# Kernel tuning notes

Hardware: AMD Instinct MI355X
Metric: run time of the kernel (lower is better)

## Reference

```python
import jax, jax.numpy as jnp
import numpy as np
import math

IMG = 256      # image H = W (img_shape)
N_ANG = 360    # projection views over [0, pi)
N_DET = 256    # radial detector bins
N_SAMP = 256   # samples along each ray
VOX = 2.0      # voxel size / detector bin width in mm (isotropic)
FWHM = 4.0     # gaussian_PSF FWHM in mm


def _gauss_kernel(sigma):
    radius = max(1, int(math.ceil(3.0 * sigma)))
    t = np.arange(-radius, radius + 1, dtype=np.float64)
    k = np.exp(-0.5 * (t / sigma) ** 2)
    return (k / k.sum()).astype(np.float32), radius


def _blur_axis(x, sigma, axis):
    """1-D Gaussian blur with reflect padding along `axis` (static small kernel)."""
    k, r = _gauss_kernel(sigma)
    x = jnp.moveaxis(x, axis, -1)
    L = x.shape[-1]
    pad = [(0, 0)] * (x.ndim - 1) + [(r, r)]
    xp = jnp.pad(x, pad, mode='reflect')
    out = sum(float(k[i]) * xp[..., i:i + L] for i in range(2 * r + 1))
    return jnp.moveaxis(out, -1, axis)


def _blur2d(x, sigma):
    return _blur_axis(_blur_axis(x, sigma, -1), sigma, -2)


def _geometry():
    """Static parallel-beam ray-sampling geometry (bilinear taps, in pixel units)."""
    theta = np.pi * np.arange(N_ANG) / N_ANG
    r = (np.arange(N_DET) - (N_DET - 1) / 2.0) * VOX   # detector offsets [mm]
    s = (np.arange(N_SAMP) - (N_SAMP - 1) / 2.0) * VOX  # depth along ray [mm]
    cos = np.cos(theta)[:, None, None]
    sin = np.sin(theta)[:, None, None]
    x = r[None, :, None] * cos - s[None, None, :] * sin  # (A, D, S) mm
    y = r[None, :, None] * sin + s[None, None, :] * cos
    ix = x / VOX + (IMG - 1) / 2.0
    iy = y / VOX + (IMG - 1) / 2.0
    valid = ((ix >= 0) & (ix <= IMG - 1) & (iy >= 0) & (iy <= IMG - 1)).astype(np.float32)
    j0 = np.clip(np.floor(ix).astype(np.int32), 0, IMG - 2)
    i0 = np.clip(np.floor(iy).astype(np.int32), 0, IMG - 2)
    fx = (ix - j0).astype(np.float32)
    fy = (iy - i0).astype(np.float32)
    return i0, j0, fy, fx, valid

_GEO = tuple(jnp.asarray(a) for a in _geometry())


def _project(img):
    """Parallel-view 2D ray projection: img (B,H,W) -> sinogram (B, N_DET, N_ANG)."""
    i0, j0, fy, fx, valid = _GEO
    v00 = img[:, i0, j0]
    v01 = img[:, i0, j0 + 1]
    v10 = img[:, i0 + 1, j0]
    v11 = img[:, i0 + 1, j0 + 1]
    vals = ((1 - fy) * (1 - fx) * v00 + (1 - fy) * fx * v01
            + fy * (1 - fx) * v10 + fy * fx * v11) * valid
    sino = vals.sum(-1) * VOX          # (B, N_ANG, N_DET), line integral in mm
    return jnp.transpose(sino, (0, 2, 1))  # (B, N_DET, N_ANG)


def setup_inputs() -> dict:
    key = jax.random.key(0)
    k1, k2 = jax.random.split(key)
    image = jax.random.uniform(k1, (2, 1, IMG, IMG), dtype=jnp.float32)
    attenuation_map = jax.random.uniform(k2, (2, 1, IMG, IMG), dtype=jnp.float32)
    return {"image": image, "attenuation_map": attenuation_map}


def reference(image, attenuation_map):
    sqrt_log2 = math.sqrt(math.log(2.0))
    sigma_img = (FWHM / (4.0 * sqrt_log2)) / VOX
    # emission PSF blur (reflect) then project
    img_b = _blur2d(image, sigma_img)
    sino = _project(img_b[:, 0])[:, None]          # (B,1,N_DET,N_ANG)
    # attenuation: wider PSF blur, 0.01 scale, project, exponential scaling
    sigma_att = (FWHM / (2.0 * sqrt_log2)) / VOX
    att_b = _blur2d(attenuation_map, sigma_att) * 0.01
    att_sino = _project(att_b[:, 0])[:, None]
    sino = sino * jnp.exp(-att_sino * VOX)
    # column-wise (detector axis) sinogram PSF
    sino = _blur_axis(sino, sigma_img, -2)
    return sino
```

## Files before the change

kernel.cpp:

```cpp
#include <hip/hip_runtime.h>
#include <math.h>

#define IMG 256
#define N_ANG 360
#define N_DET 256

#define NH_BLOCKS 181
#define NV_BLOCKS (179 * 32)
#define EPS 1e-3f

struct W9 { float w[9]; };
struct AngTab { double c, sn; float cf, snf; float pad0, pad1; };

typedef _Float16 h2 __attribute__((ext_vector_type(2)));

#if __has_builtin(__builtin_amdgcn_fdot2)
__device__ __forceinline__ float fdot2(h2 a, h2 b, float c) {
    return __builtin_amdgcn_fdot2(a, b, c, false);
}
#else
__device__ __forceinline__ float fdot2(h2 a, h2 b, float c) {
    return c + (float)a[0] * (float)b[0] + (float)a[1] * (float)b[1];
}
#endif

__device__ __forceinline__ h2 as_h2(unsigned u) { return __builtin_bit_cast(h2, u); }
__device__ __forceinline__ unsigned pack2(float a, float b) {
    h2 v = { (_Float16)a, (_Float16)b };
    return __builtin_bit_cast(unsigned, v);
}
__device__ __forceinline__ unsigned prm(unsigned hi, unsigned lo, unsigned sel) {
#if __has_builtin(__builtin_amdgcn_perm)
    return __builtin_amdgcn_perm(hi, lo, sel);
#else
    unsigned long long cat = ((unsigned long long)hi << 32) | lo;
    unsigned r = 0;
    for (int i = 0; i < 4; ++i) r |= ((unsigned)(cat >> (8 * ((sel >> (8 * i)) & 7))) & 0xff) << (8 * i);
    return r;
#endif
}

__device__ __forceinline__ int refl(int i, int L) {
    if (i < 0) i = -i;
    if (i >= L) i = 2 * (L - 1) - i;
    return i;
}

__global__ void blurpix_k(const float* __restrict__ img, const float* __restrict__ att,
                          uint2* __restrict__ pix, AngTab* __restrict__ tab,
                          W9 wi, W9 wa) {
    int x = threadIdx.x, y = blockIdx.x;
    int gid = y * IMG + x;
    if (gid < N_ANG) {
        double th = M_PI * (double)gid / 360.0;
        double c = cos(th), sn = sin(th);
        AngTab tb;
        tb.c = c; tb.sn = sn; tb.cf = (float)c; tb.snf = (float)sn;
        tb.pad0 = 0.f; tb.pad1 = 0.f;
        tab[gid] = tb;
    }
    float v[4];
    #pragma unroll
    for (int m = 0; m < 4; ++m) {
        const float* src = ((m & 1) ? att : img) + (m >> 1) * IMG * IMG;
        const float* w = (m & 1) ? wa.w : wi.w;
        float acc = 0.f;
        for (int dy = -4; dy <= 4; ++dy) {
            float wy = w[dy + 4];
            if (wy == 0.f) continue;
            const float* rowp = src + refl(y + dy, IMG) * IMG;
            float ra = 0.f;
            for (int dx = -4; dx <= 4; ++dx) ra += w[dx + 4] * rowp[refl(x + dx, IMG)];
            acc += wy * ra;
        }
        v[m] = acc * ((m & 1) ? 0.01f : 1.0f);
    }
    uint2 o;
    o.x = pack2(v[0], v[1]);
    o.y = pack2(v[2], v[3]);
    pix[gid] = o;
}

template <typename P>
__device__ __forceinline__ int lastTrue(P p) {
    if (!p(0)) return -1;
    if (p(255)) return 255;
    int lo = 0, hi = 255;
    while (lo < hi) { int m = (lo + hi + 1) >> 1; if (p(m)) lo = m; else hi = m - 1; }
    return lo;
}
template <typename P>
__device__ __forceinline__ int firstTrue(P p) {
    if (!p(255)) return 256;
    if (p(0)) return 0;
    int lo = 0, hi = 255;
    while (lo < hi) { int m = (lo + hi) >> 1; if (p(m)) hi = m; else lo = m + 1; }
    return lo;
}

__device__ __forceinline__ void tap_acc(const uint2* __restrict__ pix,
                                        int i0, int j0,
                                        float w00, float w01, float w10, float w11,
                                        float4& acc) {
    h2 wt = { (_Float16)w00, (_Float16)w01 };
    h2 wb = { (_Float16)w10, (_Float16)w11 };
    const uint2* p0 = pix + (i0 << 8) + j0;
    uint4 T = *(const uint4*)p0;
    uint4 B = *(const uint4*)(p0 + IMG);
    unsigned ti0 = prm(T.z, T.x, 0x05040100);
    unsigned ta0 = prm(T.z, T.x, 0x07060302);
    unsigned ti1 = prm(T.w, T.y, 0x05040100);
    unsigned ta1 = prm(T.w, T.y, 0x07060302);
    unsigned bi0 = prm(B.z, B.x, 0x05040100);
    unsigned ba0 = prm(B.z, B.x, 0x07060302);
    unsigned bi1 = prm(B.w, B.y, 0x05040100);
    unsigned ba1 = prm(B.w, B.y, 0x07060302);
    acc.x = fdot2(as_h2(ti0), wt, acc.x);
    acc.x = fdot2(as_h2(bi0), wb, acc.x);
    acc.y = fdot2(as_h2(ta0), wt, acc.y);
    acc.y = fdot2(as_h2(ba0), wb, acc.y);
    acc.z = fdot2(as_h2(ti1), wt, acc.z);
    acc.z = fdot2(as_h2(bi1), wb, acc.z);
    acc.w = fdot2(as_h2(ta1), wt, acc.w);
    acc.w = fdot2(as_h2(ba1), wb, acc.w);
}

__global__ __launch_bounds__(512) void proj_k(const uint2* __restrict__ pix,
                                              const AngTab* __restrict__ tab,
                                              float4* __restrict__ part4,
                                              float* __restrict__ out, W9 wblur) {
    int t = threadIdx.x;
    int bx = blockIdx.x;

    if (bx < NH_BLOCKS) {
        int d = t & 255, kc = t >> 8;
        int a = (bx <= 90) ? bx : bx + 179;
        AngTab tb = tab[a];
        double rr = (double)(2 * d - 255);
        double rc = __dmul_rn(rr, tb.c), rs = __dmul_rn(rr, tb.sn);

        auto evIx = [&](int k) -> double {
            double ss = (double)(2 * k - 255);
            return __dadd_rn(__dmul_rn(__dsub_rn(rc, __dmul_rn(ss, tb.sn)), 0.5), 127.5);
        };
        auto evIy = [&](int k) -> double {
            double ss = (double)(2 * k - 255);
            return __dadd_rn(__dmul_rn(__dadd_rn(rs, __dmul_rn(ss, tb.c)), 0.5), 127.5);
        };
        int khiA = lastTrue([&](int k) { return evIx(k) >= 0.0; });
        int kloA = firstTrue([&](int k) { return evIx(k) <= 255.0; });
        int kloB, khiB;
        if (tb.c > 0.0) {
            kloB = firstTrue([&](int k) { return evIy(k) >= 0.0; });
            khiB = lastTrue([&](int k) { return evIy(k) <= 255.0; });
        } else {
            khiB = lastTrue([&](int k) { return evIy(k) >= 0.0; });
            kloB = firstTrue([&](int k) { return evIy(k) <= 255.0; });
        }
        int lo = max(kloA, kloB), hi = min(khiA, khiB);
        lo = max(lo, kc * 128); hi = min(hi, kc * 128 + 127);
        if (lo > hi) { lo = 0; hi = -1; }

        int jl = (hi >= lo) ? lo : 0x7fffffff;
        int jh = (hi >= lo) ? hi : (-0x7fffffff - 1);
        #pragma unroll
        for (int off = 32; off; off >>= 1) {
            jl = min(jl, __shfl_xor(jl, off));
            jh = max(jh, __shfl_xor(jh, off));
        }

        float x0f = (float)evIx(128);
        float y0f = (float)evIy(128);
        float dxf = -tb.snf, dyf = tb.cf;

        float4 acc = make_float4(0.f, 0.f, 0.f, 0.f);
        for (int kb = jl; kb <= jh; kb += 4) {
            #pragma unroll
            for (int u = 0; u < 4; ++u) {
                int k = kb + u;
                float kf = (float)(k - 128);
                float ixf = fmaf(kf, dxf, x0f);
                float iyf = fmaf(kf, dyf, y0f);
                float m = (k >= lo && k <= hi) ? 2.0f : 0.0f;
                int j0 = (int)ixf; j0 = min(max(j0, 0), 254);
                int i0 = (int)iyf; i0 = min(max(i0, 0), 254);
                float fx = ixf - (float)j0;
                float fy = iyf - (float)i0;
                float gxm = (1.f - fx) * m, fxm = fx * m;
                float gy = 1.f - fy;
                tap_acc(pix, i0, j0, gy * gxm, gy * fxm, fy * gxm, fy * fxm, acc);
            }
        }

        __shared__ float4 red[512];
        __shared__ float vb[2][N_DET];
        red[t] = acc;
        __syncthreads();
        if (t < 256) {
            float4 u = red[t], v = red[t + 256];
            float si0 = u.x + v.x, sa0 = u.y + v.y;
            float si1 = u.z + v.z, sa1 = u.w + v.w;
            vb[0][t] = si0 * expf(-sa0 * 2.0f);
            vb[1][t] = si1 * expf(-sa1 * 2.0f);
        }
        __syncthreads();
        if (t < 256) {
            float a0 = 0.f, a1 = 0.f;
            #pragma unroll
            for (int i = -2; i <= 2; ++i) {
                int dd = refl(t + i, N_DET);
                a0 += wblur.w[i + 2] * vb[0][dd];
                a1 += wblur.w[i + 2] * vb[1][dd];
            }
            out[t * N_ANG + a] = a0;
            out[(N_DET + t) * N_ANG + a] = a1;
        }
    } else {
        int idx = bx - NH_BLOCKS;
        int a = 91 + (idx >> 5);
        int dgrp = idx & 31;
        int lane = t & 63, w = t >> 6;
        int d = dgrp * 8 + w;
        AngTab tb = tab[a];
        float cf = tb.cf, snf = tb.snf;
        float df = (float)d - 127.5f;
        float hx = fmaf(df, cf, 127.5f);
        float hy = fmaf(df, snf, 127.5f);

        float4 acc = make_float4(0.f, 0.f, 0.f, 0.f);
        #pragma unroll
        for (int j = 0; j < 4; ++j) {
            int k = j * 64 + lane;
            float kf = (float)k - 127.5f;
            float ixf = fmaf(-kf, snf, hx);
            float iyf = fmaf(kf, cf, hy);
            float vmin = fminf(fminf(ixf, 255.0f - ixf), fminf(iyf, 255.0f - iyf));
            if (!__any(vmin > -EPS)) continue;
            float m = (vmin >= EPS) ? 2.0f : 0.0f;
            if (fabsf(vmin) < EPS) {
                double ss = (double)(2 * k - 255);
                double rr = (double)(2 * d - 255);
                double rc = __dmul_rn(rr, tb.c), rs = __dmul_rn(rr, tb.sn);
                double ixd = __dadd_rn(__dmul_rn(__dsub_rn(rc, __dmul_rn(ss, tb.sn)), 0.5), 127.5);
                double iyd = __dadd_rn(__dmul_rn(__dadd_rn(rs, __dmul_rn(ss, tb.c)), 0.5), 127.5);
                bool v = (ixd >= 0.0) && (ixd <= 255.0) && (iyd >= 0.0) && (iyd <= 255.0);
                m = v ? 2.0f : 0.0f;
            }
            int j0 = (int)ixf; j0 = min(max(j0, 0), 254);
            int i0 = (int)iyf; i0 = min(max(i0, 0), 254);
            float fx = ixf - (float)j0;
            float fy = iyf - (float)i0;
            float gxm = (1.f - fx) * m, fxm = fx * m;
            float gy = 1.f - fy;
            tap_acc(pix, i0, j0, gy * gxm, gy * fxm, fy * gxm, fy * fxm, acc);
        }

        #pragma unroll
        for (int off = 32; off; off >>= 1) {
            acc.x += __shfl_xor(acc.x, off);
            acc.y += __shfl_xor(acc.y, off);
            acc.z += __shfl_xor(acc.z, off);
            acc.w += __shfl_xor(acc.w, off);
        }
        if (lane == 0) part4[a * N_DET + d] = acc;
    }
}

__global__ __launch_bounds__(256) void finish_v_k(const float4* __restrict__ part4,
                                                  float* __restrict__ out, W9 wt) {
    int d = threadIdx.x;
    int b = blockIdx.x / 179;
    int a = 91 + (blockIdx.x % 179);
    float4 s = part4[a * N_DET + d];
    float si = b ? s.z : s.x;
    float sa = b ? s.w : s.y;
    __shared__ float vb[N_DET];
    vb[d] = si * expf(-sa * 2.0f);
    __syncthreads();
    float acc = 0.f;
    #pragma unroll
    for (int i = -2; i <= 2; ++i) acc += wt.w[i + 2] * vb[refl(d + i, N_DET)];
    out[(b * N_DET + d) * N_ANG + a] = acc;
}

static void gauss_w(W9* wt, double sigma, int r, int pad_to_center4) {
    double tmp[9];
    double s = 0.0;
    for (int i = -r; i <= r; ++i) {
        double v = exp(-0.5 * ((double)i / sigma) * ((double)i / sigma));
        tmp[i + r] = v;
        s += v;
    }
    for (int i = 0; i < 9; ++i) wt->w[i] = 0.f;
    int off = pad_to_center4 ? (4 - r) : 0;
    for (int i = 0; i < 2 * r + 1; ++i) wt->w[i + off] = (float)(tmp[i] / s);
}

extern "C" void kernel_launch(void* const* d_in, const int* in_sizes, int n_in,
                              void* d_out, int out_size, void* d_ws, size_t ws_size,
                              hipStream_t stream) {
    const float* img = (const float*)d_in[0];
    const float* att = (const float*)d_in[1];
    float* out = (float*)d_out;

    char* ws = (char*)d_ws;
    AngTab* tab = (AngTab*)ws;
    uint2* pix = (uint2*)(ws + 16384);
    float4* part4 = (float4*)(ws + 16384 + (1 << 19));

    double sqrt_log2 = sqrt(log(2.0));
    double sigma_img = 4.0 / (4.0 * sqrt_log2) / 2.0;
    double sigma_att = 4.0 / (2.0 * sqrt_log2) / 2.0;
    W9 wimg_pad, wimg, watt;
    gauss_w(&wimg_pad, sigma_img, 2, 1);
    gauss_w(&wimg, sigma_img, 2, 0);
    gauss_w(&watt, sigma_att, 4, 0);

    blurpix_k<<<IMG, IMG, 0, stream>>>(img, att, pix, tab, wimg_pad, watt);
    proj_k<<<NH_BLOCKS + NV_BLOCKS, 512, 0, stream>>>(pix, tab, part4, out, wimg);
    finish_v_k<<<2 * 179, N_DET, 0, stream>>>(part4, out, wimg);
}
```

Before: 60.88 us.

## Store pre-paired horizontal neighbors in pixel buffer to drop byte permutes

The blur kernel now writes each pixel as a 16-byte record that holds its own fp16 values and those of its right neighbor, already paired per channel. The projection tap can then feed the loaded words straight into fdot2 and no longer needs eight perm instructions per tap. The blur loop also uses an exact radius per channel instead of skipping zero weights at runtime. In exchange, the pixel buffer doubles in size, each bilinear tap loads 32 bytes instead of 32 bytes spanning two texels, and the cache footprint grows.

```diff
diff --git a/kernel.cpp b/kernel.cpp
--- a/kernel.cpp
+++ b/kernel.cpp
@@ -29,16 +29,6 @@
     h2 v = { (_Float16)a, (_Float16)b };
     return __builtin_bit_cast(unsigned, v);
 }
-__device__ __forceinline__ unsigned prm(unsigned hi, unsigned lo, unsigned sel) {
-#if __has_builtin(__builtin_amdgcn_perm)
-    return __builtin_amdgcn_perm(hi, lo, sel);
-#else
-    unsigned long long cat = ((unsigned long long)hi << 32) | lo;
-    unsigned r = 0;
-    for (int i = 0; i < 4; ++i) r |= ((unsigned)(cat >> (8 * ((sel >> (8 * i)) & 7))) & 0xff) << (8 * i);
-    return r;
-#endif
-}
 
 __device__ __forceinline__ int refl(int i, int L) {
     if (i < 0) i = -i;
@@ -47,7 +37,7 @@
 }
 
 __global__ void blurpix_k(const float* __restrict__ img, const float* __restrict__ att,
-                          uint2* __restrict__ pix, AngTab* __restrict__ tab,
+                          uint4* __restrict__ pix2, AngTab* __restrict__ tab,
                           W9 wi, W9 wa) {
     int x = threadIdx.x, y = blockIdx.x;
     int gid = y * IMG + x;
@@ -64,21 +54,26 @@
     for (int m = 0; m < 4; ++m) {
         const float* src = ((m & 1) ? att : img) + (m >> 1) * IMG * IMG;
         const float* w = (m & 1) ? wa.w : wi.w;
+        const int r = (m & 1) ? 4 : 2;
         float acc = 0.f;
-        for (int dy = -4; dy <= 4; ++dy) {
-            float wy = w[dy + 4];
-            if (wy == 0.f) continue;
+        for (int dy = -r; dy <= r; ++dy) {
             const float* rowp = src + refl(y + dy, IMG) * IMG;
             float ra = 0.f;
-            for (int dx = -4; dx <= 4; ++dx) ra += w[dx + 4] * rowp[refl(x + dx, IMG)];
-            acc += wy * ra;
+            for (int dx = -r; dx <= r; ++dx) ra += w[dx + r] * rowp[refl(x + dx, IMG)];
+            acc += w[dy + r] * ra;
         }
         v[m] = acc * ((m & 1) ? 0.01f : 1.0f);
     }
-    uint2 o;
-    o.x = pack2(v[0], v[1]);
-    o.y = pack2(v[2], v[3]);
-    pix[gid] = o;
+    __shared__ float4 row[IMG];
+    row[x] = make_float4(v[0], v[1], v[2], v[3]);
+    __syncthreads();
+    float4 rn = row[min(x + 1, IMG - 1)];
+    uint4 o;
+    o.x = pack2(v[0], rn.x);
+    o.y = pack2(v[1], rn.y);
+    o.z = pack2(v[2], rn.z);
+    o.w = pack2(v[3], rn.w);
+    pix2[gid] = o;
 }
 
 template <typename P>
@@ -98,34 +93,26 @@
     return lo;
 }
 
-__device__ __forceinline__ void tap_acc(const uint2* __restrict__ pix,
+__device__ __forceinline__ void tap_acc(const uint4* __restrict__ pix2,
                                         int i0, int j0,
                                         float w00, float w01, float w10, float w11,
                                         float4& acc) {
     h2 wt = { (_Float16)w00, (_Float16)w01 };
     h2 wb = { (_Float16)w10, (_Float16)w11 };
-    const uint2* p0 = pix + (i0 << 8) + j0;
-    uint4 T = *(const uint4*)p0;
-    uint4 B = *(const uint4*)(p0 + IMG);
-    unsigned ti0 = prm(T.z, T.x, 0x05040100);
-    unsigned ta0 = prm(T.z, T.x, 0x07060302);
-    unsigned ti1 = prm(T.w, T.y, 0x05040100);
-    unsigned ta1 = prm(T.w, T.y, 0x07060302);
-    unsigned bi0 = prm(B.z, B.x, 0x05040100);
-    unsigned ba0 = prm(B.z, B.x, 0x07060302);
-    unsigned bi1 = prm(B.w, B.y, 0x05040100);
-    unsigned ba1 = prm(B.w, B.y, 0x07060302);
-    acc.x = fdot2(as_h2(ti0), wt, acc.x);
-    acc.x = fdot2(as_h2(bi0), wb, acc.x);
-    acc.y = fdot2(as_h2(ta0), wt, acc.y);
-    acc.y = fdot2(as_h2(ba0), wb, acc.y);
-    acc.z = fdot2(as_h2(ti1), wt, acc.z);
-    acc.z = fdot2(as_h2(bi1), wb, acc.z);
-    acc.w = fdot2(as_h2(ta1), wt, acc.w);
-    acc.w = fdot2(as_h2(ba1), wb, acc.w);
-}
-
-__global__ __launch_bounds__(512) void proj_k(const uint2* __restrict__ pix,
+    const uint4* p0 = pix2 + (i0 << 8) + j0;
+    uint4 T = p0[0];
+    uint4 B = p0[IMG];
+    acc.x = fdot2(as_h2(T.x), wt, acc.x);
+    acc.x = fdot2(as_h2(B.x), wb, acc.x);
+    acc.y = fdot2(as_h2(T.y), wt, acc.y);
+    acc.y = fdot2(as_h2(B.y), wb, acc.y);
+    acc.z = fdot2(as_h2(T.z), wt, acc.z);
+    acc.z = fdot2(as_h2(B.z), wb, acc.z);
+    acc.w = fdot2(as_h2(T.w), wt, acc.w);
+    acc.w = fdot2(as_h2(B.w), wb, acc.w);
+}
+
+__global__ __launch_bounds__(512) void proj_k(const uint4* __restrict__ pix2,
                                               const AngTab* __restrict__ tab,
                                               float4* __restrict__ part4,
                                               float* __restrict__ out, W9 wblur) {
@@ -188,7 +175,7 @@
                 float fy = iyf - (float)i0;
                 float gxm = (1.f - fx) * m, fxm = fx * m;
                 float gy = 1.f - fy;
-                tap_acc(pix, i0, j0, gy * gxm, gy * fxm, fy * gxm, fy * fxm, acc);
+                tap_acc(pix2, i0, j0, gy * gxm, gy * fxm, fy * gxm, fy * fxm, acc);
             }
         }
 
@@ -252,7 +239,7 @@
             float fy = iyf - (float)i0;
             float gxm = (1.f - fx) * m, fxm = fx * m;
             float gy = 1.f - fy;
-            tap_acc(pix, i0, j0, gy * gxm, gy * fxm, fy * gxm, fy * fxm, acc);
+            tap_acc(pix2, i0, j0, gy * gxm, gy * fxm, fy * gxm, fy * fxm, acc);
         }
 
         #pragma unroll
@@ -283,7 +270,7 @@
     out[(b * N_DET + d) * N_ANG + a] = acc;
 }
 
-static void gauss_w(W9* wt, double sigma, int r, int pad_to_center4) {
+static void gauss_w(W9* wt, double sigma, int r) {
     double tmp[9];
     double s = 0.0;
     for (int i = -r; i <= r; ++i) {
@@ -292,8 +279,7 @@
         s += v;
     }
     for (int i = 0; i < 9; ++i) wt->w[i] = 0.f;
-    int off = pad_to_center4 ? (4 - r) : 0;
-    for (int i = 0; i < 2 * r + 1; ++i) wt->w[i + off] = (float)(tmp[i] / s);
+    for (int i = 0; i < 2 * r + 1; ++i) wt->w[i] = (float)(tmp[i] / s);
 }
 
 extern "C" void kernel_launch(void* const* d_in, const int* in_sizes, int n_in,
@@ -305,18 +291,17 @@
 
     char* ws = (char*)d_ws;
     AngTab* tab = (AngTab*)ws;
-    uint2* pix = (uint2*)(ws + 16384);
-    float4* part4 = (float4*)(ws + 16384 + (1 << 19));
+    uint4* pix2 = (uint4*)(ws + 16384);
+    float4* part4 = (float4*)(ws + 16384 + (1 << 20));
 
     double sqrt_log2 = sqrt(log(2.0));
     double sigma_img = 4.0 / (4.0 * sqrt_log2) / 2.0;
     double sigma_att = 4.0 / (2.0 * sqrt_log2) / 2.0;
-    W9 wimg_pad, wimg, watt;
-    gauss_w(&wimg_pad, sigma_img, 2, 1);
-    gauss_w(&wimg, sigma_img, 2, 0);
-    gauss_w(&watt, sigma_att, 4, 0);
-
-    blurpix_k<<<IMG, IMG, 0, stream>>>(img, att, pix, tab, wimg_pad, watt);
-    proj_k<<<NH_BLOCKS + NV_BLOCKS, 512, 0, stream>>>(pix, tab, part4, out, wimg);
+    W9 wimg, watt;
+    gauss_w(&wimg, sigma_img, 2);
+    gauss_w(&watt, sigma_att, 4);
+
+    blurpix_k<<<IMG, IMG, 0, stream>>>(img, att, pix2, tab, wimg, watt);
+    proj_k<<<NH_BLOCKS + NV_BLOCKS, 512, 0, stream>>>(pix2, tab, part4, out, wimg);
     finish_v_k<<<2 * 179, N_DET, 0, stream>>>(part4, out, wimg);
 }
```

Result: faster. 58.07 us, median of 2 (-4.6%).
